# Kernel tuning notes

Hardware: AMD Instinct MI355X
Metric: run time of the kernel (lower is better)

## Reference

```python
import math
import jax, jax.numpy as jnp
import numpy as np

NUM_HEADS = 16
NEG_INF = -1e30


def setup_inputs() -> dict:
    key = jax.random.key(0)
    k1, k2, k3, k4 = jax.random.split(key, 4)
    B, C, T = 4, 1024, 2048
    x = jax.random.normal(k1, (B, C, T), dtype=jnp.float32)
    mask = jax.random.randint(k2, (B, T), 0, 2, dtype=jnp.int32)
    # kernel-size-1 Conv1d with bias=False == matmul; torch init scale ~ 1/sqrt(fan_in)
    W_mem = jax.random.normal(k3, (2 * C, C), dtype=jnp.float32) / math.sqrt(C)
    W_q = jax.random.normal(k4, (C, C), dtype=jnp.float32) / math.sqrt(C)
    return {"x": x, "mask": mask, "W_mem": W_mem, "W_q": W_q}


def reference(x, mask, W_mem, W_q):
    B, C, T = x.shape
    nh = NUM_HEADS
    dh = C // nh
    # kernel-size-1 conv projections, output already transposed to [B, T, ch]
    memory = jnp.einsum('oc,bct->bto', W_mem, x)   # [B, T, 2C]
    query = jnp.einsum('oc,bct->bto', W_q, x)      # [B, T, C]
    Q = query.reshape(B, T, nh, dh).transpose(0, 2, 1, 3)           # [B, nh, T, dh]
    Km, Vm = jnp.split(memory, 2, axis=-1)
    K = Km.reshape(B, T, nh, dh).transpose(0, 2, 1, 3)              # [B, nh, T, dh]
    V = Vm.reshape(B, T, nh, dh).transpose(0, 2, 1, 3)              # [B, nh, T, dh]
    att = jnp.einsum('bhqd,bhkd->bhqk', Q, K) * (1.0 / math.sqrt(dh))
    m = mask.reshape(B, 1, 1, T).astype(att.dtype)
    logits = m * att + (1.0 - m) * NEG_INF  # masked_softmax convention
    weights = jax.nn.softmax(logits, axis=-1)
    # dropout is identity in eval mode
    out = jnp.einsum('bhqk,bhkd->bhqd', weights, V)                 # [B, nh, T, dh]
    return out.transpose(0, 2, 1, 3).reshape(B, T, C).transpose(0, 2, 1)  # [B, C, T]
```

## Files before the change

### kernel.cpp

```cpp
#include <hip/hip_runtime.h>

#define B_ 4
#define C_ 1024
#define T_ 2048
#define NH 16
#define DH 64
#define TC 3072

typedef __attribute__((ext_vector_type(8))) short short8;
typedef __attribute__((ext_vector_type(4))) short short4v;
typedef __attribute__((ext_vector_type(4))) float f32x4;
typedef __attribute__((ext_vector_type(16))) float f32x16;
typedef __attribute__((ext_vector_type(2))) unsigned int u32x2;
typedef __attribute__((ext_vector_type(4))) unsigned int u32x4;

#define S2Q 0.1803368801111204f

static __device__ __forceinline__ unsigned short f2bf(float f){
  unsigned int u = __builtin_bit_cast(unsigned int, f);
  u += 0x7fffu + ((u >> 16) & 1u);
  return (unsigned short)(u >> 16);
}

__global__ __launch_bounds__(256) void cast_w_kernel(const float* __restrict__ Wmem,
                                                     const float* __restrict__ Wq,
                                                     unsigned short* __restrict__ Wc){
  size_t base = ((size_t)blockIdx.x*256 + threadIdx.x)*4;
  float4 v;
  if (base < (size_t)2048*1024) v = *(const float4*)(Wmem + base);
  else                          v = *(const float4*)(Wq + (base - (size_t)2048*1024));
  short4v o;
  o.x = (short)f2bf(v.x); o.y = (short)f2bf(v.y);
  o.z = (short)f2bf(v.z); o.w = (short)f2bf(v.w);
  *(short4v*)(Wc + base) = o;
}

__global__ __launch_bounds__(256) void mask_bias_kernel(const int* __restrict__ mask,
                                                        float* __restrict__ fbias){
  int i = blockIdx.x*256 + threadIdx.x;
  fbias[i] = mask[i] ? 0.f : -1e30f;
}

__global__ __launch_bounds__(256) void transpose_x_kernel(const float* __restrict__ x,
                                                          unsigned short* __restrict__ xT){
  __shared__ float tile[32][33];
  int b = blockIdx.z;
  int c0 = blockIdx.y*32, t0 = blockIdx.x*32;
  int tx = threadIdx.x, ty = threadIdx.y;
  const float* xp = x + ((size_t)b*C_ + c0)*T_ + t0;
  #pragma unroll
  for (int i=0;i<4;i++) tile[ty+8*i][tx] = xp[(size_t)(ty+8*i)*T_ + tx];
  __syncthreads();
  unsigned short* op = xT + ((size_t)b*T_ + t0)*C_ + c0;
  int cp = tx & 15, tw = tx >> 4;
  #pragma unroll
  for (int i=0;i<2;i++){
    int trow = ty + 8*tw + 16*i;
    unsigned int pk = (unsigned int)f2bf(tile[2*cp][trow])
                    | ((unsigned int)f2bf(tile[2*cp+1][trow]) << 16);
    *(unsigned int*)(op + (size_t)trow*C_ + 2*cp) = pk;
  }
}

#define PBM 128
#define PBN 128
#define PBK 64

__global__ __launch_bounds__(256) void proj_gemm_kernel(const unsigned short* __restrict__ Wc,
    const unsigned short* __restrict__ xT,
    unsigned short* __restrict__ Kb, unsigned short* __restrict__ Vt,
    unsigned short* __restrict__ Qb){
  __shared__ unsigned short sA[PBM*PBK];
  __shared__ unsigned short sB[PBN*PBK];
  int b = blockIdx.y;
  int nbn = T_/PBN;
  int o0 = (int)(blockIdx.x / nbn)*PBM;
  int t0 = (int)(blockIdx.x % nbn)*PBN;
  int tid = threadIdx.x;
  int lane = tid & 63, wave = tid >> 6;
  int wr = wave >> 1, wc = wave & 1;
  f32x4 acc[4][4] = {};
  const unsigned short* Abase = Wc + (size_t)o0*C_;
  const unsigned short* Bbase = xT + ((size_t)b*T_ + t0)*C_;
  auto ldsA = (__attribute__((address_space(3))) char*)sA;
  auto ldsB = (__attribute__((address_space(3))) char*)sB;
  for (int k0=0; k0<C_; k0+=PBK){
    #pragma unroll
    for (int i=0;i<4;i++){
      int L  = wave*4096 + i*1024;
      int Ll = L + lane*16;
      int row = Ll >> 7;
      int jb  = Ll & 127;
      const char* srcA = (const char*)(Abase + (size_t)row*C_ + k0) + jb;
      const char* srcB = (const char*)(Bbase + (size_t)row*C_ + k0) + jb;
      __builtin_amdgcn_global_load_lds((const __attribute__((address_space(1))) void*)srcA,
                                       (__attribute__((address_space(3))) void*)(ldsA + L), 16, 0, 0);
      __builtin_amdgcn_global_load_lds((const __attribute__((address_space(1))) void*)srcB,
                                       (__attribute__((address_space(3))) void*)(ldsB + L), 16, 0, 0);
    }
    __syncthreads();
    #pragma unroll
    for (int ks=0; ks<2; ks++){
      short8 af[4], bfr[4];
      #pragma unroll
      for (int m=0;m<4;m++){
        int row = wr*64 + m*16 + (lane & 15);
        af[m] = *(const short8*)((const char*)sA + row*128 + ks*64 + ((lane>>4)*16));
      }
      #pragma unroll
      for (int n=0;n<4;n++){
        int row = wc*64 + n*16 + (lane & 15);
        bfr[n] = *(const short8*)((const char*)sB + row*128 + ks*64 + ((lane>>4)*16));
      }
      #pragma unroll
      for (int m=0;m<4;m++){
        #pragma unroll
        for (int n=0;n<4;n++)
          acc[m][n] = __builtin_amdgcn_mfma_f32_16x16x32_bf16(af[m], bfr[n], acc[m][n], 0, 0, 0);
      }
    }
    __syncthreads();
  }
  int rowbase = o0 + wr*64;
  #pragma unroll
  for (int m=0;m<4;m++){
    int o = rowbase + m*16 + ((lane>>4)*4);
    #pragma unroll
    for (int n=0;n<4;n++){
      int t = t0 + wc*64 + n*16 + (lane & 15);
      f32x4 v = acc[m][n];
      if (o < C_){
        int h = o >> 6, d = o & 63;
        unsigned short* p = Kb + (((size_t)(b*NH + h)*T_ + t)*DH + d);
        short4v s; s.x=(short)f2bf(v.x); s.y=(short)f2bf(v.y);
        s.z=(short)f2bf(v.z); s.w=(short)f2bf(v.w);
        *(short4v*)p = s;
      } else if (o < 2*C_){
        int oo = o - C_;
        int h = oo >> 6, d = oo & 63;
        unsigned short* p = Vt + (((size_t)(b*NH + h)*DH + d)*T_ + t);
        p[0]    = f2bf(v.x);
        p[T_]   = f2bf(v.y);
        p[2*T_] = f2bf(v.z);
        p[3*T_] = f2bf(v.w);
      } else {
        int oo = o - 2*C_;
        int h = oo >> 6, d = oo & 63;
        unsigned short* p = Qb + (((size_t)(b*NH + h)*T_ + t)*DH + d);
        short4v s; s.x=(short)f2bf(v.x*S2Q); s.y=(short)f2bf(v.y*S2Q);
        s.z=(short)f2bf(v.z*S2Q); s.w=(short)f2bf(v.w*S2Q);
        *(short4v*)p = s;
      }
    }
  }
}

#define KB_ 64

#define GLL(SRC, SHBUF, LOFF) \
  __builtin_amdgcn_global_load_lds((const __attribute__((address_space(1))) void*)(SRC), \
      (__attribute__((address_space(3))) void*)((__attribute__((address_space(3))) char*)(SHBUF) + (LOFF)), 16, 0, 0)

#define MAX3(a,b,c) fmaxf(fmaxf((a),(b)),(c))

#define TILE(CBUF, POFF, DOSTAGE) do {                                                 \
  union { f32x4 q[4]; f32x16 v; } cb0, cb1;                                            \
  _Pragma("unroll")                                                                    \
  for (int m=0;m<4;m++){                                                               \
    cb0.q[m] = *(const f32x4*)(bptr + (POFF) + m*8);                                   \
    cb1.q[m] = *(const f32x4*)(bptr + (POFF) + 32 + m*8);                              \
  }                                                                                    \
  if (DOSTAGE) {                                                                       \
    GLL(srcK0, &sK[(CBUF)^1][0], L0);                                                  \
    GLL(srcK1, &sK[(CBUF)^1][0], L0 + 1024);                                           \
    GLL(srcV0, &sV[(CBUF)^1][0], L0);                                                  \
    GLL(srcV1, &sV[(CBUF)^1][0], L0 + 1024);                                           \
    srcK0 += 8192; srcK1 += 8192; srcV0 += 128; srcV1 += 128;                          \
    asm volatile("s_waitcnt vmcnt(12)" ::: "memory");                                  \
  } else {                                                                             \
    asm volatile("s_waitcnt vmcnt(8)" ::: "memory");                                   \
  }                                                                                    \
  __builtin_amdgcn_s_barrier();                                                        \
  __builtin_amdgcn_sched_barrier(0);                                                   \
  const char* sKb = (const char*)&sK[CBUF][0] + l31*128;                               \
  const char* sVb = (const char*)&sV[CBUF][0] + l31*128;                               \
  f32x16 s0 = cb0.v, s1 = cb1.v;                                                       \
  _Pragma("unroll")                                                                    \
  for (int kc=0;kc<4;kc++){                                                            \
    int co = (((kc<<1)|h) ^ rsw) << 4;                                                 \
    short8 kf0 = *(const short8*)(sKb + co);                                           \
    short8 kf1 = *(const short8*)(sKb + 4096 + co);                                    \
    s0 = __builtin_amdgcn_mfma_f32_32x32x16_bf16(kf0, qf[kc], s0, 0,0,0);              \
    s1 = __builtin_amdgcn_mfma_f32_32x32x16_bf16(kf1, qf[kc], s1, 0,0,0);              \
  }                                                                                    \
  float t0_ = MAX3(s0[0],s0[1],s0[2]),   t1_ = MAX3(s0[3],s0[4],s0[5]);                \
  float t2_ = MAX3(s0[6],s0[7],s0[8]),   t3_ = MAX3(s0[9],s0[10],s0[11]);              \
  float t4_ = MAX3(s0[12],s0[13],s0[14]), t5_ = MAX3(s0[15],s1[0],s1[1]);              \
  float t6_ = MAX3(s1[2],s1[3],s1[4]),   t7_ = MAX3(s1[5],s1[6],s1[7]);                \
  float t8_ = MAX3(s1[8],s1[9],s1[10]),  t9_ = MAX3(s1[11],s1[12],s1[13]);             \
  float u0_ = MAX3(t0_,t1_,t2_), u1_ = MAX3(t3_,t4_,t5_);                              \
  float u2_ = MAX3(t6_,t7_,t8_), u3_ = MAX3(t9_,s1[14],s1[15]);                        \
  float pmax = MAX3(MAX3(u0_,u1_,u2_), u3_, -1e30f);                                   \
  if (!__all(pmax - mrun <= 8.0f)){                                                    \
    float pm = fmaxf(pmax, __shfl_xor(pmax, 32));                                      \
    float mnew = fmaxf(mrun, pm);                                                      \
    float alpha = __builtin_amdgcn_exp2f(mrun - mnew);                                 \
    mrun = mnew; lpart *= alpha;                                                       \
    _Pragma("unroll")                                                                  \
    for (int r=0;r<16;r++){                                                            \
      float ar = __shfl(alpha, (r&3) + 8*(r>>2) + 4*h);                                \
      acco0[r] *= ar; acco1[r] *= ar;                                                  \
    }                                                                                  \
  }                                                                                    \
  float ps_ = 0.f;                                                                     \
  _Pragma("unroll")                                                                    \
  for (int j=0;j<16;j++){                                                              \
    s0[j] = __builtin_amdgcn_exp2f(s0[j] - mrun); ps_ += s0[j];                        \
    s1[j] = __builtin_amdgcn_exp2f(s1[j] - mrun); ps_ += s1[j];                        \
  }                                                                                    \
  lpart += ps_;                                                                        \
  unsigned int Wp[2][4][2];                                                            \
  _Pragma("unroll")                                                                    \
  for (int m=0;m<4;m++){                                                               \
    asm volatile("v_cvt_pk_bf16_f32 %0, %1, %2" : "=v"(Wp[0][m][0]) : "v"(s0[4*m]),   "v"(s0[4*m+1]));  \
    asm volatile("v_cvt_pk_bf16_f32 %0, %1, %2" : "=v"(Wp[0][m][1]) : "v"(s0[4*m+2]), "v"(s0[4*m+3]));  \
    asm volatile("v_cvt_pk_bf16_f32 %0, %1, %2" : "=v"(Wp[1][m][0]) : "v"(s1[4*m]),   "v"(s1[4*m+1]));  \
    asm volatile("v_cvt_pk_bf16_f32 %0, %1, %2" : "=v"(Wp[1][m][1]) : "v"(s1[4*m+2]), "v"(s1[4*m+3]));  \
  }                                                                                    \
  _Pragma("unroll")                                                                    \
  for (int kb=0;kb<2;kb++){                                                            \
    _Pragma("unroll")                                                                  \
    for (int e=0;e<2;e++){                                                             \
      u32x2 x0 = __builtin_amdgcn_permlane32_swap(Wp[kb][2*e][0], Wp[kb][2*e+1][0], 0, 0); \
      u32x2 x1 = __builtin_amdgcn_permlane32_swap(Wp[kb][2*e][1], Wp[kb][2*e+1][1], 0, 0); \
      u32x4 pw; pw.x = x0.x; pw.y = x1.x; pw.z = x0.y; pw.w = x1.y;                    \
      short8 pf = __builtin_bit_cast(short8, pw);                                      \
      int vo = (((((kb<<1)|e)<<1)|h) ^ rsw) << 4;                                      \
      short8 vf0 = *(const short8*)(sVb + vo);                                         \
      short8 vf1 = *(const short8*)(sVb + 4096 + vo);                                  \
      acco0 = __builtin_amdgcn_mfma_f32_32x32x16_bf16(pf, vf0, acco0, 0,0,0);          \
      acco1 = __builtin_amdgcn_mfma_f32_32x32x16_bf16(pf, vf1, acco1, 0,0,0);          \
    }                                                                                  \
  }                                                                                    \
  __builtin_amdgcn_sched_barrier(0);                                                   \
  __builtin_amdgcn_s_barrier();                                                        \
} while(0)

__global__ __launch_bounds__(256) void attn_kernel(const unsigned short* __restrict__ Qb,
    const unsigned short* __restrict__ Kb, const unsigned short* __restrict__ Vt,
    const float* __restrict__ fbias, float* __restrict__ out){
  __shared__ unsigned short sK[2][KB_*DH];
  __shared__ unsigned short sV[2][KB_*DH];
  const int Lid = blockIdx.x;
  const int xcd = Lid & 7, jj = Lid >> 3;
  const int bh = ((jj & 7) << 3) | xcd;
  const int qblk = jj >> 3;
  const int b = bh >> 4;
  const int tid = threadIdx.x, lane = tid & 63, wave = tid >> 6;
  const int l31 = lane & 31, h = lane >> 5;
  const int rsw = l31 & 7;
  const unsigned short* Kbase = Kb + (size_t)bh*T_*DH;
  const unsigned short* Vbase = Vt + (size_t)bh*DH*T_;
  const float* bptr = fbias + (size_t)b*T_ + 4*h;
  const int qrow = qblk*128 + wave*32 + l31;
  const unsigned short* Qp = Qb + ((size_t)bh*T_ + qrow)*DH + h*8;
  short8 qf[4];
  #pragma unroll
  for (int kc=0;kc<4;kc++) qf[kc] = *(const short8*)(Qp + kc*16);
  f32x16 acco0 = {}, acco1 = {};
  float mrun = -1e30f, lpart = 0.f;
  const int L0  = wave*2048;
  const int Ll0 = L0 + lane*16, Ll1 = Ll0 + 1024;
  const int row0 = Ll0 >> 7, row1 = Ll1 >> 7;
  const int cg0 = ((Ll0 >> 4) & 7) ^ (row0 & 7);
  const int cg1 = ((Ll1 >> 4) & 7) ^ (row1 & 7);
  const char* srcK0 = (const char*)Kbase + row0*128 + cg0*16;
  const char* srcK1 = (const char*)Kbase + row1*128 + cg1*16;
  const char* srcV0 = (const char*)Vbase + (size_t)row0*(T_*2) + cg0*16;
  const char* srcV1 = (const char*)Vbase + (size_t)row1*(T_*2) + cg1*16;

  GLL(srcK0, &sK[0][0], L0);
  GLL(srcK1, &sK[0][0], L0 + 1024);
  GLL(srcV0, &sV[0][0], L0);
  GLL(srcV1, &sV[0][0], L0 + 1024);
  srcK0 += 8192; srcK1 += 8192; srcV0 += 128; srcV1 += 128;
  __syncthreads();

  for (int kt2 = 0; kt2 < T_/KB_/2 - 1; kt2++){
    TILE(0,  0, true);
    TILE(1, 64, true);
    bptr += 128;
  }
  TILE(0,  0, true);
  TILE(1, 64, false);

  lpart += __shfl_xor(lpart, 32);
  float inv = 1.0f / lpart;
  const int head = bh & 15;
  const int qbase = qblk*128 + wave*32;
  #pragma unroll
  for (int m=0;m<4;m++){
    float rv[4];
    #pragma unroll
    for (int s=0;s<4;s++) rv[s] = __shfl(inv, 8*m + 4*h + s);
    int t = qbase + 8*m + 4*h;
    float4 v0, v1;
    v0.x = acco0[4*m+0]*rv[0]; v0.y = acco0[4*m+1]*rv[1];
    v0.z = acco0[4*m+2]*rv[2]; v0.w = acco0[4*m+3]*rv[3];
    v1.x = acco1[4*m+0]*rv[0]; v1.y = acco1[4*m+1]*rv[1];
    v1.z = acco1[4*m+2]*rv[2]; v1.w = acco1[4*m+3]*rv[3];
    size_t off0 = ((size_t)b*C_ + head*64 + l31)*T_ + t;
    size_t off1 = ((size_t)b*C_ + head*64 + 32 + l31)*T_ + t;
    *(float4*)(out + off0) = v0;
    *(float4*)(out + off1) = v1;
  }
}

extern "C" void kernel_launch(void* const* d_in, const int* in_sizes, int n_in,
                              void* d_out, int out_size, void* d_ws, size_t ws_size,
                              hipStream_t stream) {
  const float* x    = (const float*)d_in[0];
  const int*   mask = (const int*)d_in[1];
  const float* Wmem = (const float*)d_in[2];
  const float* Wq   = (const float*)d_in[3];
  float* out = (float*)d_out;

  unsigned short* ws = (unsigned short*)d_ws;
  unsigned short* xT = ws;
  unsigned short* Wc = xT + (size_t)B_*T_*C_;
  unsigned short* Qb = Wc + (size_t)TC*C_;
  unsigned short* Kb = Qb + (size_t)B_*NH*T_*DH;
  unsigned short* Vt = Kb + (size_t)B_*NH*T_*DH;
  float* fbias = (float*)(Vt + (size_t)B_*NH*T_*DH);

  cast_w_kernel<<<dim3(TC*C_/1024), dim3(256), 0, stream>>>(Wmem, Wq, Wc);
  mask_bias_kernel<<<dim3(B_*T_/256), dim3(256), 0, stream>>>(mask, fbias);
  transpose_x_kernel<<<dim3(T_/32, C_/32, B_), dim3(32,8), 0, stream>>>(x, xT);
  proj_gemm_kernel<<<dim3((TC/PBM)*(T_/PBN), B_), dim3(256), 0, stream>>>(Wc, xT, Kb, Vt, Qb);
  attn_kernel<<<dim3((T_/128)*(B_*NH)), dim3(256), 0, stream>>>(Qb, Kb, Vt, fbias, out);
}
```

Measured before the change: 200.9 us.

## Compact unmasked keys via prefix scan and skip masked K/V work

A per-batch prefix scan over the mask builds a list of the unmasked key positions and their count. The K/V projection GEMM gathers only those rows of x, so key/value tiles beyond the padded count are never computed. The attention loop then runs over only the compacted tiles. With a random 0/1 mask this roughly halves both the K/V projection and the attention work. In exchange it adds a serial scan kernel, gather-indexed loads in the GEMM, and a runtime loop bound in the attention kernel.

```diff
diff --git a/kernel.cpp b/kernel.cpp
--- a/kernel.cpp
+++ b/kernel.cpp
@@ -35,10 +35,39 @@
   *(short4v*)(Wc + base) = o;
 }
 
-__global__ __launch_bounds__(256) void mask_bias_kernel(const int* __restrict__ mask,
-                                                        float* __restrict__ fbias){
-  int i = blockIdx.x*256 + threadIdx.x;
-  fbias[i] = mask[i] ? 0.f : -1e30f;
+__global__ __launch_bounds__(256) void scan_mask_kernel(const int* __restrict__ mask,
+    int* __restrict__ idx, int* __restrict__ nkinfo, float* __restrict__ cbias){
+  __shared__ int cnt[256];
+  int b = blockIdx.x;
+  int tid = threadIdx.x;
+  const int* mb = mask + (size_t)b*T_;
+  int base = tid*8;
+  int m[8]; int c = 0;
+  #pragma unroll
+  for (int i=0;i<8;i++){ m[i] = mb[base+i]; c += m[i]; }
+  cnt[tid] = c;
+  __syncthreads();
+  for (int off=1; off<256; off<<=1){
+    int v = (tid >= off) ? cnt[tid-off] : 0;
+    __syncthreads();
+    cnt[tid] += v;
+    __syncthreads();
+  }
+  int nk  = cnt[255];
+  int pos = cnt[tid] - c;
+  #pragma unroll
+  for (int i=0;i<8;i++){
+    if (m[i]) idx[(size_t)b*T_ + (pos++)] = base + i;
+  }
+  #pragma unroll
+  for (int i=0;i<8;i++){
+    int j = base + i;
+    cbias[(size_t)b*T_ + j] = (j < nk) ? 0.f : -1e30f;
+  }
+  if (tid == 0){
+    nkinfo[b]   = (nk + 127) & ~127;
+    nkinfo[4+b] = nk;
+  }
 }
 
 __global__ __launch_bounds__(256) void transpose_x_kernel(const float* __restrict__ x,
@@ -67,7 +96,8 @@
 #define PBK 64
 
 __global__ __launch_bounds__(256) void proj_gemm_kernel(const unsigned short* __restrict__ Wc,
-    const unsigned short* __restrict__ xT,
+    const unsigned short* __restrict__ xT, const int* __restrict__ idx,
+    const int* __restrict__ nkinfo,
     unsigned short* __restrict__ Kb, unsigned short* __restrict__ Vt,
     unsigned short* __restrict__ Qb){
   __shared__ unsigned short sA[PBM*PBK];
@@ -76,14 +106,29 @@
   int nbn = T_/PBN;
   int o0 = (int)(blockIdx.x / nbn)*PBM;
   int t0 = (int)(blockIdx.x % nbn)*PBN;
+  const bool isKV = (o0 < 2*C_);
+  const int nk128 = nkinfo[b], nk = nkinfo[4+b];
+  if (isKV && t0 >= nk128) return;
   int tid = threadIdx.x;
   int lane = tid & 63, wave = tid >> 6;
   int wr = wave >> 1, wc = wave & 1;
   f32x4 acc[4][4] = {};
   const unsigned short* Abase = Wc + (size_t)o0*C_;
-  const unsigned short* Bbase = xT + ((size_t)b*T_ + t0)*C_;
+  const unsigned short* xTb = xT + (size_t)b*T_*C_;
   auto ldsA = (__attribute__((address_space(3))) char*)sA;
   auto ldsB = (__attribute__((address_space(3))) char*)sB;
+  const char* srcBrow[4];
+  #pragma unroll
+  for (int i=0;i<4;i++){
+    int L  = wave*4096 + i*1024;
+    int Ll = L + lane*16;
+    int row = Ll >> 7;
+    int jb  = Ll & 127;
+    int trow = t0 + row;
+    int grow = trow;
+    if (isKV) grow = (trow < nk) ? idx[(size_t)b*T_ + trow] : 0;
+    srcBrow[i] = (const char*)(xTb + (size_t)grow*C_) + jb;
+  }
   for (int k0=0; k0<C_; k0+=PBK){
     #pragma unroll
     for (int i=0;i<4;i++){
@@ -92,7 +137,7 @@
       int row = Ll >> 7;
       int jb  = Ll & 127;
       const char* srcA = (const char*)(Abase + (size_t)row*C_ + k0) + jb;
-      const char* srcB = (const char*)(Bbase + (size_t)row*C_ + k0) + jb;
+      const char* srcB = srcBrow[i] + (size_t)k0*2;
       __builtin_amdgcn_global_load_lds((const __attribute__((address_space(1))) void*)srcA,
                                        (__attribute__((address_space(3))) void*)(ldsA + L), 16, 0, 0);
       __builtin_amdgcn_global_load_lds((const __attribute__((address_space(1))) void*)srcB,
@@ -163,92 +208,10 @@
 
 #define MAX3(a,b,c) fmaxf(fmaxf((a),(b)),(c))
 
-#define TILE(CBUF, POFF, DOSTAGE) do {                                                 \
-  union { f32x4 q[4]; f32x16 v; } cb0, cb1;                                            \
-  _Pragma("unroll")                                                                    \
-  for (int m=0;m<4;m++){                                                               \
-    cb0.q[m] = *(const f32x4*)(bptr + (POFF) + m*8);                                   \
-    cb1.q[m] = *(const f32x4*)(bptr + (POFF) + 32 + m*8);                              \
-  }                                                                                    \
-  if (DOSTAGE) {                                                                       \
-    GLL(srcK0, &sK[(CBUF)^1][0], L0);                                                  \
-    GLL(srcK1, &sK[(CBUF)^1][0], L0 + 1024);                                           \
-    GLL(srcV0, &sV[(CBUF)^1][0], L0);                                                  \
-    GLL(srcV1, &sV[(CBUF)^1][0], L0 + 1024);                                           \
-    srcK0 += 8192; srcK1 += 8192; srcV0 += 128; srcV1 += 128;                          \
-    asm volatile("s_waitcnt vmcnt(12)" ::: "memory");                                  \
-  } else {                                                                             \
-    asm volatile("s_waitcnt vmcnt(8)" ::: "memory");                                   \
-  }                                                                                    \
-  __builtin_amdgcn_s_barrier();                                                        \
-  __builtin_amdgcn_sched_barrier(0);                                                   \
-  const char* sKb = (const char*)&sK[CBUF][0] + l31*128;                               \
-  const char* sVb = (const char*)&sV[CBUF][0] + l31*128;                               \
-  f32x16 s0 = cb0.v, s1 = cb1.v;                                                       \
-  _Pragma("unroll")                                                                    \
-  for (int kc=0;kc<4;kc++){                                                            \
-    int co = (((kc<<1)|h) ^ rsw) << 4;                                                 \
-    short8 kf0 = *(const short8*)(sKb + co);                                           \
-    short8 kf1 = *(const short8*)(sKb + 4096 + co);                                    \
-    s0 = __builtin_amdgcn_mfma_f32_32x32x16_bf16(kf0, qf[kc], s0, 0,0,0);              \
-    s1 = __builtin_amdgcn_mfma_f32_32x32x16_bf16(kf1, qf[kc], s1, 0,0,0);              \
-  }                                                                                    \
-  float t0_ = MAX3(s0[0],s0[1],s0[2]),   t1_ = MAX3(s0[3],s0[4],s0[5]);                \
-  float t2_ = MAX3(s0[6],s0[7],s0[8]),   t3_ = MAX3(s0[9],s0[10],s0[11]);              \
-  float t4_ = MAX3(s0[12],s0[13],s0[14]), t5_ = MAX3(s0[15],s1[0],s1[1]);              \
-  float t6_ = MAX3(s1[2],s1[3],s1[4]),   t7_ = MAX3(s1[5],s1[6],s1[7]);                \
-  float t8_ = MAX3(s1[8],s1[9],s1[10]),  t9_ = MAX3(s1[11],s1[12],s1[13]);             \
-  float u0_ = MAX3(t0_,t1_,t2_), u1_ = MAX3(t3_,t4_,t5_);                              \
-  float u2_ = MAX3(t6_,t7_,t8_), u3_ = MAX3(t9_,s1[14],s1[15]);                        \
-  float pmax = MAX3(MAX3(u0_,u1_,u2_), u3_, -1e30f);                                   \
-  if (!__all(pmax - mrun <= 8.0f)){                                                    \
-    float pm = fmaxf(pmax, __shfl_xor(pmax, 32));                                      \
-    float mnew = fmaxf(mrun, pm);                                                      \
-    float alpha = __builtin_amdgcn_exp2f(mrun - mnew);                                 \
-    mrun = mnew; lpart *= alpha;                                                       \
-    _Pragma("unroll")                                                                  \
-    for (int r=0;r<16;r++){                                                            \
-      float ar = __shfl(alpha, (r&3) + 8*(r>>2) + 4*h);                                \
-      acco0[r] *= ar; acco1[r] *= ar;                                                  \
-    }                                                                                  \
-  }                                                                                    \
-  float ps_ = 0.f;                                                                     \
-  _Pragma("unroll")                                                                    \
-  for (int j=0;j<16;j++){                                                              \
-    s0[j] = __builtin_amdgcn_exp2f(s0[j] - mrun); ps_ += s0[j];                        \
-    s1[j] = __builtin_amdgcn_exp2f(s1[j] - mrun); ps_ += s1[j];                        \
-  }                                                                                    \
-  lpart += ps_;                                                                        \
-  unsigned int Wp[2][4][2];                                                            \
-  _Pragma("unroll")                                                                    \
-  for (int m=0;m<4;m++){                                                               \
-    asm volatile("v_cvt_pk_bf16_f32 %0, %1, %2" : "=v"(Wp[0][m][0]) : "v"(s0[4*m]),   "v"(s0[4*m+1]));  \
-    asm volatile("v_cvt_pk_bf16_f32 %0, %1, %2" : "=v"(Wp[0][m][1]) : "v"(s0[4*m+2]), "v"(s0[4*m+3]));  \
-    asm volatile("v_cvt_pk_bf16_f32 %0, %1, %2" : "=v"(Wp[1][m][0]) : "v"(s1[4*m]),   "v"(s1[4*m+1]));  \
-    asm volatile("v_cvt_pk_bf16_f32 %0, %1, %2" : "=v"(Wp[1][m][1]) : "v"(s1[4*m+2]), "v"(s1[4*m+3]));  \
-  }                                                                                    \
-  _Pragma("unroll")                                                                    \
-  for (int kb=0;kb<2;kb++){                                                            \
-    _Pragma("unroll")                                                                  \
-    for (int e=0;e<2;e++){                                                             \
-      u32x2 x0 = __builtin_amdgcn_permlane32_swap(Wp[kb][2*e][0], Wp[kb][2*e+1][0], 0, 0); \
-      u32x2 x1 = __builtin_amdgcn_permlane32_swap(Wp[kb][2*e][1], Wp[kb][2*e+1][1], 0, 0); \
-      u32x4 pw; pw.x = x0.x; pw.y = x1.x; pw.z = x0.y; pw.w = x1.y;                    \
-      short8 pf = __builtin_bit_cast(short8, pw);                                      \
-      int vo = (((((kb<<1)|e)<<1)|h) ^ rsw) << 4;                                      \
-      short8 vf0 = *(const short8*)(sVb + vo);                                         \
-      short8 vf1 = *(const short8*)(sVb + 4096 + vo);                                  \
-      acco0 = __builtin_amdgcn_mfma_f32_32x32x16_bf16(pf, vf0, acco0, 0,0,0);          \
-      acco1 = __builtin_amdgcn_mfma_f32_32x32x16_bf16(pf, vf1, acco1, 0,0,0);          \
-    }                                                                                  \
-  }                                                                                    \
-  __builtin_amdgcn_sched_barrier(0);                                                   \
-  __builtin_amdgcn_s_barrier();                                                        \
-} while(0)
-
 __global__ __launch_bounds__(256) void attn_kernel(const unsigned short* __restrict__ Qb,
     const unsigned short* __restrict__ Kb, const unsigned short* __restrict__ Vt,
-    const float* __restrict__ fbias, float* __restrict__ out){
+    const float* __restrict__ cbias, const int* __restrict__ nkinfo,
+    float* __restrict__ out){
   __shared__ unsigned short sK[2][KB_*DH];
   __shared__ unsigned short sV[2][KB_*DH];
   const int Lid = blockIdx.x;
@@ -256,12 +219,13 @@
   const int bh = ((jj & 7) << 3) | xcd;
   const int qblk = jj >> 3;
   const int b = bh >> 4;
+  const int ntiles = nkinfo[b] >> 6;
   const int tid = threadIdx.x, lane = tid & 63, wave = tid >> 6;
   const int l31 = lane & 31, h = lane >> 5;
   const int rsw = l31 & 7;
   const unsigned short* Kbase = Kb + (size_t)bh*T_*DH;
   const unsigned short* Vbase = Vt + (size_t)bh*DH*T_;
-  const float* bptr = fbias + (size_t)b*T_ + 4*h;
+  const float* bptr = cbias + (size_t)b*T_ + 4*h;
   const int qrow = qblk*128 + wave*32 + l31;
   const unsigned short* Qp = Qb + ((size_t)bh*T_ + qrow)*DH + h*8;
   short8 qf[4];
@@ -286,13 +250,91 @@
   srcK0 += 8192; srcK1 += 8192; srcV0 += 128; srcV1 += 128;
   __syncthreads();
 
-  for (int kt2 = 0; kt2 < T_/KB_/2 - 1; kt2++){
-    TILE(0,  0, true);
-    TILE(1, 64, true);
-    bptr += 128;
-  }
-  TILE(0,  0, true);
-  TILE(1, 64, false);
+  for (int kt = 0; kt < ntiles; kt++){
+    const int cb = kt & 1;
+    union { f32x4 q[4]; f32x16 v; } cb0, cb1;
+    #pragma unroll
+    for (int m=0;m<4;m++){
+      cb0.q[m] = *(const f32x4*)(bptr + m*8);
+      cb1.q[m] = *(const f32x4*)(bptr + 32 + m*8);
+    }
+    bptr += 64;
+    if (kt + 1 < ntiles){
+      int db = cb ^ 1;
+      GLL(srcK0, &sK[0][0], db*8192 + L0);
+      GLL(srcK1, &sK[0][0], db*8192 + L0 + 1024);
+      GLL(srcV0, &sV[0][0], db*8192 + L0);
+      GLL(srcV1, &sV[0][0], db*8192 + L0 + 1024);
+      srcK0 += 8192; srcK1 += 8192; srcV0 += 128; srcV1 += 128;
+      asm volatile("s_waitcnt vmcnt(12)" ::: "memory");
+    } else {
+      asm volatile("s_waitcnt vmcnt(8)" ::: "memory");
+    }
+    __builtin_amdgcn_s_barrier();
+    __builtin_amdgcn_sched_barrier(0);
+    const char* sKb = (const char*)&sK[0][0] + cb*8192 + l31*128;
+    const char* sVb = (const char*)&sV[0][0] + cb*8192 + l31*128;
+    f32x16 s0 = cb0.v, s1 = cb1.v;
+    #pragma unroll
+    for (int kc=0;kc<4;kc++){
+      int co = (((kc<<1)|h) ^ rsw) << 4;
+      short8 kf0 = *(const short8*)(sKb + co);
+      short8 kf1 = *(const short8*)(sKb + 4096 + co);
+      s0 = __builtin_amdgcn_mfma_f32_32x32x16_bf16(kf0, qf[kc], s0, 0,0,0);
+      s1 = __builtin_amdgcn_mfma_f32_32x32x16_bf16(kf1, qf[kc], s1, 0,0,0);
+    }
+    float t0_ = MAX3(s0[0],s0[1],s0[2]),   t1_ = MAX3(s0[3],s0[4],s0[5]);
+    float t2_ = MAX3(s0[6],s0[7],s0[8]),   t3_ = MAX3(s0[9],s0[10],s0[11]);
+    float t4_ = MAX3(s0[12],s0[13],s0[14]), t5_ = MAX3(s0[15],s1[0],s1[1]);
+    float t6_ = MAX3(s1[2],s1[3],s1[4]),   t7_ = MAX3(s1[5],s1[6],s1[7]);
+    float t8_ = MAX3(s1[8],s1[9],s1[10]),  t9_ = MAX3(s1[11],s1[12],s1[13]);
+    float u0_ = MAX3(t0_,t1_,t2_), u1_ = MAX3(t3_,t4_,t5_);
+    float u2_ = MAX3(t6_,t7_,t8_), u3_ = MAX3(t9_,s1[14],s1[15]);
+    float pmax = MAX3(MAX3(u0_,u1_,u2_), u3_, -1e30f);
+    if (!__all(pmax - mrun <= 8.0f)){
+      float pm = fmaxf(pmax, __shfl_xor(pmax, 32));
+      float mnew = fmaxf(mrun, pm);
+      float alpha = __builtin_amdgcn_exp2f(mrun - mnew);
+      mrun = mnew; lpart *= alpha;
+      #pragma unroll
+      for (int r=0;r<16;r++){
+        float ar = __shfl(alpha, (r&3) + 8*(r>>2) + 4*h);
+        acco0[r] *= ar; acco1[r] *= ar;
+      }
+    }
+    float ps_ = 0.f;
+    #pragma unroll
+    for (int j=0;j<16;j++){
+      s0[j] = __builtin_amdgcn_exp2f(s0[j] - mrun); ps_ += s0[j];
+      s1[j] = __builtin_amdgcn_exp2f(s1[j] - mrun); ps_ += s1[j];
+    }
+    lpart += ps_;
+    unsigned int Wp[2][4][2];
+    #pragma unroll
+    for (int m=0;m<4;m++){
+      asm volatile("v_cvt_pk_bf16_f32 %0, %1, %2" : "=v"(Wp[0][m][0]) : "v"(s0[4*m]),   "v"(s0[4*m+1]));
+      asm volatile("v_cvt_pk_bf16_f32 %0, %1, %2" : "=v"(Wp[0][m][1]) : "v"(s0[4*m+2]), "v"(s0[4*m+3]));
+      asm volatile("v_cvt_pk_bf16_f32 %0, %1, %2" : "=v"(Wp[1][m][0]) : "v"(s1[4*m]),   "v"(s1[4*m+1]));
+      asm volatile("v_cvt_pk_bf16_f32 %0, %1, %2" : "=v"(Wp[1][m][1]) : "v"(s1[4*m+2]), "v"(s1[4*m+3]));
+    }
+    #pragma unroll
+    for (int kb=0;kb<2;kb++){
+      #pragma unroll
+      for (int e=0;e<2;e++){
+        u32x2 x0 = __builtin_amdgcn_permlane32_swap(Wp[kb][2*e][0], Wp[kb][2*e+1][0], 0, 0);
+        u32x2 x1 = __builtin_amdgcn_permlane32_swap(Wp[kb][2*e][1], Wp[kb][2*e+1][1], 0, 0);
+        u32x4 pw; pw.x = x0.x; pw.y = x1.x; pw.z = x0.y; pw.w = x1.y;
+        short8 pf = __builtin_bit_cast(short8, pw);
+        int vo = (((((kb<<1)|e)<<1)|h) ^ rsw) << 4;
+        short8 vf0 = *(const short8*)(sVb + vo);
+        short8 vf1 = *(const short8*)(sVb + 4096 + vo);
+        acco0 = __builtin_amdgcn_mfma_f32_32x32x16_bf16(pf, vf0, acco0, 0,0,0);
+        acco1 = __builtin_amdgcn_mfma_f32_32x32x16_bf16(pf, vf1, acco1, 0,0,0);
+      }
+    }
+    __builtin_amdgcn_sched_barrier(0);
+    __builtin_amdgcn_s_barrier();
+  }
 
   lpart += __shfl_xor(lpart, 32);
   float inv = 1.0f / lpart;
@@ -331,11 +373,13 @@
   unsigned short* Qb = Wc + (size_t)TC*C_;
   unsigned short* Kb = Qb + (size_t)B_*NH*T_*DH;
   unsigned short* Vt = Kb + (size_t)B_*NH*T_*DH;
-  float* fbias = (float*)(Vt + (size_t)B_*NH*T_*DH);
+  float* cbias = (float*)(Vt + (size_t)B_*NH*T_*DH);
+  int*   idx   = (int*)(cbias + (size_t)B_*T_);
+  int*   nkinfo = idx + (size_t)B_*T_;
 
   cast_w_kernel<<<dim3(TC*C_/1024), dim3(256), 0, stream>>>(Wmem, Wq, Wc);
-  mask_bias_kernel<<<dim3(B_*T_/256), dim3(256), 0, stream>>>(mask, fbias);
+  scan_mask_kernel<<<dim3(B_), dim3(256), 0, stream>>>(mask, idx, nkinfo, cbias);
   transpose_x_kernel<<<dim3(T_/32, C_/32, B_), dim3(32,8), 0, stream>>>(x, xT);
-  proj_gemm_kernel<<<dim3((TC/PBM)*(T_/PBN), B_), dim3(256), 0, stream>>>(Wc, xT, Kb, Vt, Qb);
-  attn_kernel<<<dim3((T_/128)*(B_*NH)), dim3(256), 0, stream>>>(Qb, Kb, Vt, fbias, out);
-}
+  proj_gemm_kernel<<<dim3((TC/PBM)*(T_/PBN), B_), dim3(256), 0, stream>>>(Wc, xT, idx, nkinfo, Kb, Vt, Qb);
+  attn_kernel<<<dim3((T_/128)*(B_*NH)), dim3(256), 0, stream>>>(Qb, Kb, Vt, cbias, nkinfo, out);
+}
```

Result: faster. 169.7 us (-15.5%).
